# Kernel optimization log

Hardware: AMD Instinct MI355X
Metric: run time of the kernel (lower is better)

## Reference

```python
import jax, jax.numpy as jnp
import numpy as np

N_UNITS = 100
N_INPUTS = 7
N_OUTPUTS = 1
T = 60
STIM_ON, STIM_OFF = 10, 15
RESP_START, RESP_END = 20, 35
REWARD_DURATION = 5
ALPHA = 0.2            # dt / tau = 100 / 500
SIGMA_REC = 0.15
B = 8192


def setup_inputs() -> dict:
    key = jax.random.key(0)
    k1, k2, k3, k4, k5, k6, k7 = jax.random.split(key, 7)
    W_in_raw = (jax.random.normal(k1, (N_UNITS, N_INPUTS)) * 0.05).astype(jnp.float32)
    W_rec_np = np.asarray(jax.random.normal(k2, (N_UNITS, N_UNITS))) / np.sqrt(N_UNITS)
    sr = float(np.abs(np.linalg.eigvals(W_rec_np)).max())
    W_rec = jnp.asarray(W_rec_np * (0.8 / sr), dtype=jnp.float32)
    b_rec = jnp.zeros((N_UNITS,), jnp.float32)
    w_out = (jax.random.normal(k3, (N_OUTPUTS, N_UNITS)) * 0.1).astype(jnp.float32)
    b_out = jnp.zeros((N_OUTPUTS,), jnp.float32)
    return {
        "y0": jnp.zeros((B, N_UNITS), jnp.float32),
        "noise": jax.random.normal(k4, (B, T, N_UNITS), dtype=jnp.float32),
        "stimulus_idx": jax.random.randint(k5, (B,), 0, 4).astype(jnp.int32),
        "rewarded_target_idx": jax.random.randint(k6, (B,), 0, 4).astype(jnp.int32),
        "instruction": jax.random.randint(k7, (B,), 0, 2).astype(jnp.int32),
        "W_in_raw": W_in_raw, "W_rec": W_rec, "b_rec": b_rec,
        "w_out": w_out, "b_out": b_out,
    }


def reference(y0, noise, stimulus_idx, rewarded_target_idx, instruction,
              W_in_raw, W_rec, b_rec, w_out, b_out):
    W_in = jnp.abs(W_in_raw)               # [N, n_in]
    w_lick = W_in[:, 5]
    w_reward = W_in[:, 4]
    noise_scale = SIGMA_REC * float(np.sqrt(2.0 * ALPHA))
    t_idx = jnp.arange(T, dtype=jnp.int32)
    stim_mask = ((t_idx >= STIM_ON) & (t_idx < STIM_OFF)).astype(jnp.float32)
    resp_mask = ((t_idx >= RESP_START) & (t_idx < RESP_END)).astype(jnp.float32)
    auto_start = RESP_END - REWARD_DURATION

    def trial(y0_i, eps_i, stim, rew, instr):
        is_rew = stim == rew
        instr_b = instr > 0
        # base open-loop input: stimulus channel + response cue (channel 6)
        u_base = jnp.zeros((T, N_INPUTS), jnp.float32).at[:, 6].set(resp_mask)
        u_base = u_base + stim_mask[:, None] * jax.nn.one_hot(stim, N_INPUTS, dtype=jnp.float32)
        wu = u_base @ W_in.T + b_rec        # [T, N]

        def step(carry, xs):
            y, licked, lick_t, instr_fired = carry
            t, wu_t, eps_t = xs
            # instruction auto-reward fires at auto_start if no reward yet (applied BEFORE pre)
            delivered = instr_fired | (licked & is_rew)
            fire = instr_b & (~delivered) & (t == auto_start)
            instr_fired = instr_fired | fire
            instr_active = instr_fired & (t >= auto_start) & (t < RESP_END)
            # lick-triggered inputs affect dynamics only AFTER the lick step (wu[t] already consumed)
            lick_dyn = licked & (t > lick_t) & (t < lick_t + REWARD_DURATION)
            add = (instr_active.astype(jnp.float32) + (lick_dyn & is_rew).astype(jnp.float32)) * w_reward \
                  + lick_dyn.astype(jnp.float32) * w_lick
            pre = y @ W_rec.T + wu_t + add + noise_scale * eps_t
            y = (1.0 - ALPHA) * y + ALPHA * jax.nn.relu(pre)
            z = jax.nn.sigmoid(y @ w_out.T + b_out)[0]
            # closed-loop lick decision (after readout)
            in_resp = (t >= RESP_START) & (t < RESP_END)
            trig = in_resp & (~licked) & (z > 0.5)
            lick_t = jnp.where(trig, t, lick_t)
            licked = licked | trig
            # u_trial markings include the lick step itself
            u5 = licked & (t >= lick_t) & (t < lick_t + REWARD_DURATION)
            u4 = instr_active | (u5 & is_rew)
            return (y, licked, lick_t, instr_fired), (z, u5, u4)

        init = (y0_i, jnp.array(False), jnp.array(T + 1, jnp.int32), jnp.array(False))
        (yf, licked, lick_t, instr_fired), (z_seq, u5, u4) = jax.lax.scan(
            step, init, (t_idx, wu, eps_i))
        u = u_base.at[:, 5].set(u5.astype(jnp.float32)).at[:, 4].set(u4.astype(jnp.float32))
        reward_delivered = instr_fired | (licked & is_rew)
        target = jnp.where(is_rew, resp_mask, jnp.zeros_like(resp_mask))
        return u, target, resp_mask > 0, licked, reward_delivered, z_seq, yf

    return jax.vmap(trial)(y0, noise, stimulus_idx, rewarded_target_idx, instruction)
```

## Files before the change

kernel.cpp:

```cpp
#include <hip/hip_runtime.h>
#include <math.h>

#define BB 8192
#define TT 60
#define NU 100
#define NI 7

typedef float v2f __attribute__((ext_vector_type(2)));
typedef float v4f __attribute__((ext_vector_type(4)));

#define FOR50(M) M(0) M(1) M(2) M(3) M(4) M(5) M(6) M(7) M(8) M(9) \
  M(10) M(11) M(12) M(13) M(14) M(15) M(16) M(17) M(18) M(19) \
  M(20) M(21) M(22) M(23) M(24) M(25) M(26) M(27) M(28) M(29) \
  M(30) M(31) M(32) M(33) M(34) M(35) M(36) M(37) M(38) M(39) \
  M(40) M(41) M(42) M(43) M(44) M(45) M(46) M(47) M(48) M(49)

#define FOR25(M) M(0,0,1) M(1,2,3) M(2,4,5) M(3,6,7) M(4,8,9) \
  M(5,10,11) M(6,12,13) M(7,14,15) M(8,16,17) M(9,18,19) \
  M(10,20,21) M(11,22,23) M(12,24,25) M(13,26,27) M(14,28,29) \
  M(15,30,31) M(16,32,33) M(17,34,35) M(18,36,37) M(19,38,39) \
  M(20,40,41) M(21,42,43) M(22,44,45) M(23,46,47) M(24,48,49)

#define DECLW(j) \
  const v2f wa_##j = rowA[j]; \
  const v2f wb_##j = rowB[j];

#define MAC2(j2, ja, jb) { \
  const v4f y4 = Yv[j2]; \
  const v2f ylo = { y4.x, y4.y }; \
  const v2f yhi = { y4.z, y4.w }; \
  accA0 += ylo * wa_##ja; \
  accB0 += ylo * wb_##ja; \
  accA1 += yhi * wa_##jb; \
  accB1 += yhi * wb_##jb; }

#define RL(v,l) __int_as_float(__builtin_amdgcn_readlane(__float_as_int(v), l))

#define DPPADD(ctrl, rmask) { \
  const int _t = __builtin_amdgcn_update_dpp(0, __float_as_int(part), (ctrl), (rmask), 0xf, false); \
  part += __int_as_float(_t); }

__global__ __launch_bounds__(256, 1)
void drr_kernel(const float* __restrict__ y0,
                const float* __restrict__ noise,
                const int*   __restrict__ stim_idx,
                const int*   __restrict__ rew_idx,
                const int*   __restrict__ instr_in,
                const float* __restrict__ W_in_raw,
                const float* __restrict__ W_rec,
                const float* __restrict__ b_rec,
                const float* __restrict__ w_out,
                const float* __restrict__ b_out,
                float* __restrict__ out)
{
    const int lane  = threadIdx.x & 63;
    const int wid   = threadIdx.x >> 6;
    const int trial = blockIdx.x * 4 + wid;

    const bool act = (lane < 50);
    const int  la  = act ? lane : 49;
    const int  ua  = 2 * la;
    const int  uao = ua * NU;

    const int  stim    = stim_idx[trial];
    const int  rew     = rew_idx[trial];
    const bool is_rew  = (stim == rew);
    const bool instr_b = (instr_in[trial] > 0);

    const v2f* rowA = (const v2f*)(W_rec + uao);
    const v2f* rowB = rowA + (NU / 2);
    FOR50(DECLW)

    const v2f wi6 = { fabsf(W_in_raw[ua * NI + 6]),    fabsf(W_in_raw[(ua+1) * NI + 6]) };
    const v2f wis = { fabsf(W_in_raw[ua * NI + stim]), fabsf(W_in_raw[(ua+1) * NI + stim]) };
    const v2f wr  = { fabsf(W_in_raw[ua * NI + 4]),    fabsf(W_in_raw[(ua+1) * NI + 4]) };
    const v2f wl  = { fabsf(W_in_raw[ua * NI + 5]),    fabsf(W_in_raw[(ua+1) * NI + 5]) };
    const v2f br  = { b_rec[ua], b_rec[ua + 1] };
    const v2f wo  = act ? (v2f){ w_out[ua], w_out[ua + 1] } : (v2f){ 0.0f, 0.0f };
    const float bo = b_out[0];

    const v2f* y0v = (const v2f*)(y0 + trial * NU);
    v2f yy = y0v[la];

    const float NS = 0.09486832980505138f;

    bool licked = false, instr_fired = false;
    int  lick_t = TT + 1;

    const float* nbase = noise + trial * (TT * NU);
    v2f en = ((const v2f*)nbase)[la];

    __shared__ v4f lds_y[4][32];
    v2f*       yw = (v2f*)&lds_y[wid][0];
    const v4f* Yv = &lds_y[wid][0];

    float* uout  = out;
    float* tout  = out  + BB * TT * NI;
    float* rout  = tout + BB * TT;
    float* lout  = rout + BB * TT;
    float* dout  = lout + BB;
    float* zout  = dout + BB;
    float* yfout = zout + BB * TT;

    for (int t = 0; t < TT; ++t) {
        yw[la] = yy;

        const v2f e = en;
        if (t < TT - 1)
            en = ((const v2f*)(nbase + (t + 1) * NU))[la];

        const float sm = (t >= 10 && t < 15) ? 1.0f : 0.0f;
        const float rm = (t >= 20 && t < 35) ? 1.0f : 0.0f;

        const bool delivered    = instr_fired || (licked && is_rew);
        const bool fire         = instr_b && !delivered && (t == 30);
        instr_fired             = instr_fired || fire;
        const bool instr_active = instr_fired && (t >= 30) && (t < 35);
        const bool lick_dyn     = licked && (t > lick_t) && (t < lick_t + 5);
        const float a_rew  = (instr_active ? 1.0f : 0.0f) + ((lick_dyn && is_rew) ? 1.0f : 0.0f);
        const float a_lick = lick_dyn ? 1.0f : 0.0f;

        const v2f base = br + rm * wi6 + sm * wis + a_rew * wr + a_lick * wl + NS * e;

        v2f accA0 = { 0.0f, 0.0f };
        v2f accA1 = { 0.0f, 0.0f };
        v2f accB0 = { 0.0f, 0.0f };
        v2f accB1 = { 0.0f, 0.0f };

        FOR25(MAC2)

        const v2f sA  = accA0 + accA1;
        const v2f sB  = accB0 + accB1;
        const v2f pre = base + (v2f){ sA.x + sA.y, sB.x + sB.y };
        const v2f prer = { fmaxf(pre.x, 0.0f), fmaxf(pre.y, 0.0f) };
        yy = 0.8f * yy + 0.2f * prer;

        float part = yy.x * wo.x + yy.y * wo.y;
        DPPADD(0x111, 0xf)
        DPPADD(0x112, 0xf)
        DPPADD(0x114, 0xf)
        DPPADD(0x118, 0xf)
        DPPADD(0x142, 0xa)
        DPPADD(0x143, 0xc)
        const float x = RL(part, 63) + bo;
        const float z = 1.0f / (1.0f + expf(-x));

        const bool in_resp = (t >= 20) && (t < 35);
        const bool trig    = in_resp && !licked && (z > 0.5f);
        if (trig) lick_t = t;
        licked = licked || trig;
        const bool u5 = licked && (t >= lick_t) && (t < lick_t + 5);
        const bool u4 = instr_active || (u5 && is_rew);

        const int bt = trial * TT + t;
        if (lane < NI) {
            float uv = 0.0f;
            if (lane == stim) uv = sm;
            if (lane == 4)    uv = u4 ? 1.0f : 0.0f;
            if (lane == 5)    uv = u5 ? 1.0f : 0.0f;
            if (lane == 6)    uv = rm;
            uout[bt * NI + lane] = uv;
        } else if (lane == 8) {
            tout[bt] = is_rew ? rm : 0.0f;
        } else if (lane == 9) {
            rout[bt] = rm;
        } else if (lane == 10) {
            zout[bt] = z;
        }
    }

    if (lane == 0) {
        lout[trial] = licked ? 1.0f : 0.0f;
        dout[trial] = (instr_fired || (licked && is_rew)) ? 1.0f : 0.0f;
    }
    if (act)
        ((v2f*)(yfout + trial * NU))[la] = yy;
}

extern "C" void kernel_launch(void* const* d_in, const int* in_sizes, int n_in,
                              void* d_out, int out_size, void* d_ws, size_t ws_size,
                              hipStream_t stream) {
    const float* y0       = (const float*)d_in[0];
    const float* noise    = (const float*)d_in[1];
    const int*   stim     = (const int*)  d_in[2];
    const int*   rew      = (const int*)  d_in[3];
    const int*   instr    = (const int*)  d_in[4];
    const float* W_in_raw = (const float*)d_in[5];
    const float* W_rec    = (const float*)d_in[6];
    const float* b_rec    = (const float*)d_in[7];
    const float* w_out    = (const float*)d_in[8];
    const float* b_out    = (const float*)d_in[9];
    float* out = (float*)d_out;

    drr_kernel<<<BB / 4, 256, 0, stream>>>(y0, noise, stim, rew, instr,
                                           W_in_raw, W_rec, b_rec, w_out, b_out, out);
}
```

Before: 519.5 us.

## Split recurrent matvec K-dimension across two waves per trial with LDS exchange

Each trial now uses two wavefronts, each holding half of the W_rec columns (50 instead of 100 per lane-pair), so register pressure drops and launch bounds allow 3 blocks per CU. Partial sums are exchanged through a double-buffered LDS array with a block-wide barrier every timestep, and the y vector is stored rotated so each half reads its own slice. Only one wave of each pair writes outputs. The trade-off is twice the launched waves and one __syncthreads per step on the serial recurrence, in exchange for higher occupancy.

```diff
diff --git a/kernel.cpp b/kernel.cpp
--- a/kernel.cpp
+++ b/kernel.cpp
@@ -9,17 +9,12 @@
 typedef float v2f __attribute__((ext_vector_type(2)));
 typedef float v4f __attribute__((ext_vector_type(4)));
 
-#define FOR50(M) M(0) M(1) M(2) M(3) M(4) M(5) M(6) M(7) M(8) M(9) \
+#define FOR25(M) M(0) M(1) M(2) M(3) M(4) M(5) M(6) M(7) M(8) M(9) \
   M(10) M(11) M(12) M(13) M(14) M(15) M(16) M(17) M(18) M(19) \
-  M(20) M(21) M(22) M(23) M(24) M(25) M(26) M(27) M(28) M(29) \
-  M(30) M(31) M(32) M(33) M(34) M(35) M(36) M(37) M(38) M(39) \
-  M(40) M(41) M(42) M(43) M(44) M(45) M(46) M(47) M(48) M(49)
-
-#define FOR25(M) M(0,0,1) M(1,2,3) M(2,4,5) M(3,6,7) M(4,8,9) \
-  M(5,10,11) M(6,12,13) M(7,14,15) M(8,16,17) M(9,18,19) \
-  M(10,20,21) M(11,22,23) M(12,24,25) M(13,26,27) M(14,28,29) \
-  M(15,30,31) M(16,32,33) M(17,34,35) M(18,36,37) M(19,38,39) \
-  M(20,40,41) M(21,42,43) M(22,44,45) M(23,46,47) M(24,48,49)
+  M(20) M(21) M(22) M(23) M(24)
+
+#define FOR12P(M) M(0,0,1) M(1,2,3) M(2,4,5) M(3,6,7) M(4,8,9) M(5,10,11) \
+  M(6,12,13) M(7,14,15) M(8,16,17) M(9,18,19) M(10,20,21) M(11,22,23)
 
 #define DECLW(j) \
   const v2f wa_##j = rowA[j]; \
@@ -40,7 +35,7 @@
   const int _t = __builtin_amdgcn_update_dpp(0, __float_as_int(part), (ctrl), (rmask), 0xf, false); \
   part += __int_as_float(_t); }
 
-__global__ __launch_bounds__(256, 1)
+__global__ __launch_bounds__(256, 3)
 void drr_kernel(const float* __restrict__ y0,
                 const float* __restrict__ noise,
                 const int*   __restrict__ stim_idx,
@@ -55,7 +50,8 @@
 {
     const int lane  = threadIdx.x & 63;
     const int wid   = threadIdx.x >> 6;
-    const int trial = blockIdx.x * 4 + wid;
+    const int kh    = wid & 1;
+    const int trial = blockIdx.x * 2 + (wid >> 1);
 
     const bool act = (lane < 50);
     const int  la  = act ? lane : 49;
@@ -67,9 +63,9 @@
     const bool is_rew  = (stim == rew);
     const bool instr_b = (instr_in[trial] > 0);
 
-    const v2f* rowA = (const v2f*)(W_rec + uao);
-    const v2f* rowB = rowA + (NU / 2);
-    FOR50(DECLW)
+    const v2f* rowA = (const v2f*)(W_rec + uao + kh * 50);
+    const v2f* rowB = (const v2f*)(W_rec + uao + NU + kh * 50);
+    FOR25(DECLW)
 
     const v2f wi6 = { fabsf(W_in_raw[ua * NI + 6]),    fabsf(W_in_raw[(ua+1) * NI + 6]) };
     const v2f wis = { fabsf(W_in_raw[ua * NI + stim]), fabsf(W_in_raw[(ua+1) * NI + stim]) };
@@ -91,8 +87,12 @@
     v2f en = ((const v2f*)nbase)[la];
 
     __shared__ v4f lds_y[4][32];
+    __shared__ v2f lds_p[2][4][64];
+
     v2f*       yw = (v2f*)&lds_y[wid][0];
     const v4f* Yv = &lds_y[wid][0];
+    const v2f* Yt = (const v2f*)&lds_y[wid][0];
+    const int  ypos = (la + kh * 25) % 50;
 
     float* uout  = out;
     float* tout  = out  + BB * TT * NI;
@@ -103,7 +103,7 @@
     float* yfout = zout + BB * TT;
 
     for (int t = 0; t < TT; ++t) {
-        yw[la] = yy;
+        yw[ypos] = yy;
 
         const v2f e = en;
         if (t < TT - 1)
@@ -127,11 +127,22 @@
         v2f accB0 = { 0.0f, 0.0f };
         v2f accB1 = { 0.0f, 0.0f };
 
-        FOR25(MAC2)
-
-        const v2f sA  = accA0 + accA1;
-        const v2f sB  = accB0 + accB1;
-        const v2f pre = base + (v2f){ sA.x + sA.y, sB.x + sB.y };
+        FOR12P(MAC2)
+        {
+            const v2f yt = Yt[24];
+            accA1 += yt * wa_24;
+            accB1 += yt * wb_24;
+        }
+
+        const v2f sA = accA0 + accA1;
+        const v2f sB = accB0 + accB1;
+        const v2f partial = { sA.x + sA.y, sB.x + sB.y };
+
+        lds_p[t & 1][wid][la] = partial;
+        __syncthreads();
+        const v2f other = lds_p[t & 1][wid ^ 1][la];
+
+        const v2f pre  = base + partial + other;
         const v2f prer = { fmaxf(pre.x, 0.0f), fmaxf(pre.y, 0.0f) };
         yy = 0.8f * yy + 0.2f * prer;
 
@@ -152,29 +163,33 @@
         const bool u5 = licked && (t >= lick_t) && (t < lick_t + 5);
         const bool u4 = instr_active || (u5 && is_rew);
 
-        const int bt = trial * TT + t;
-        if (lane < NI) {
-            float uv = 0.0f;
-            if (lane == stim) uv = sm;
-            if (lane == 4)    uv = u4 ? 1.0f : 0.0f;
-            if (lane == 5)    uv = u5 ? 1.0f : 0.0f;
-            if (lane == 6)    uv = rm;
-            uout[bt * NI + lane] = uv;
-        } else if (lane == 8) {
-            tout[bt] = is_rew ? rm : 0.0f;
-        } else if (lane == 9) {
-            rout[bt] = rm;
-        } else if (lane == 10) {
-            zout[bt] = z;
+        if (kh == 0) {
+            const int bt = trial * TT + t;
+            if (lane < NI) {
+                float uv = 0.0f;
+                if (lane == stim) uv = sm;
+                if (lane == 4)    uv = u4 ? 1.0f : 0.0f;
+                if (lane == 5)    uv = u5 ? 1.0f : 0.0f;
+                if (lane == 6)    uv = rm;
+                uout[bt * NI + lane] = uv;
+            } else if (lane == 8) {
+                tout[bt] = is_rew ? rm : 0.0f;
+            } else if (lane == 9) {
+                rout[bt] = rm;
+            } else if (lane == 10) {
+                zout[bt] = z;
+            }
         }
     }
 
-    if (lane == 0) {
-        lout[trial] = licked ? 1.0f : 0.0f;
-        dout[trial] = (instr_fired || (licked && is_rew)) ? 1.0f : 0.0f;
+    if (kh == 0) {
+        if (lane == 0) {
+            lout[trial] = licked ? 1.0f : 0.0f;
+            dout[trial] = (instr_fired || (licked && is_rew)) ? 1.0f : 0.0f;
+        }
+        if (act)
+            ((v2f*)(yfout + trial * NU))[la] = yy;
     }
-    if (act)
-        ((v2f*)(yfout + trial * NU))[la] = yy;
 }
 
 extern "C" void kernel_launch(void* const* d_in, const int* in_sizes, int n_in,
@@ -192,6 +207,6 @@
     const float* b_out    = (const float*)d_in[9];
     float* out = (float*)d_out;
 
-    drr_kernel<<<BB / 4, 256, 0, stream>>>(y0, noise, stim, rew, instr,
+    drr_kernel<<<BB / 2, 256, 0, stream>>>(y0, noise, stim, rew, instr,
                                            W_in_raw, W_rec, b_rec, w_out, b_out, out);
 }
```

Measured after the change: 635.8 us. +22.4%, slower.

## Process two trials per wavefront and software-pipeline readout with next step

Applied to the files above, without the earlier changes.

Each wavefront now advances two independent trials at once, reusing the register-resident W_rec rows for both. The grid is halved. The sigmoid/lick decision and output stores for step t-1 are deferred and interleaved with step t's matvec, so the serial DPP reduction and readlane latency overlap with independent work. This adds more accumulators and live state per lane, which raises register pressure. It also halves the number of wavefronts, reducing latency hiding through occupancy.

```diff
diff --git a/kernel.cpp b/kernel.cpp
--- a/kernel.cpp
+++ b/kernel.cpp
@@ -8,6 +8,7 @@
 
 typedef float v2f __attribute__((ext_vector_type(2)));
 typedef float v4f __attribute__((ext_vector_type(4)));
+
 
 #define FOR50(M) M(0) M(1) M(2) M(3) M(4) M(5) M(6) M(7) M(8) M(9) \
   M(10) M(11) M(12) M(13) M(14) M(15) M(16) M(17) M(18) M(19) \
@@ -25,20 +26,75 @@
   const v2f wa_##j = rowA[j]; \
   const v2f wb_##j = rowB[j];
 
-#define MAC2(j2, ja, jb) { \
-  const v4f y4 = Yv[j2]; \
-  const v2f ylo = { y4.x, y4.y }; \
-  const v2f yhi = { y4.z, y4.w }; \
-  accA0 += ylo * wa_##ja; \
-  accB0 += ylo * wb_##ja; \
-  accA1 += yhi * wa_##jb; \
-  accB1 += yhi * wb_##jb; }
+#define MACJ(j2, ja, jb) { \
+  const v4f yA4 = YvA[j2]; \
+  const v4f yB4 = YvB[j2]; \
+  acc0A += (v2f){yA4.x, yA4.y} * wa_##ja; \
+  acc1A += (v2f){yA4.x, yA4.y} * wb_##ja; \
+  acc2A += (v2f){yA4.z, yA4.w} * wa_##jb; \
+  acc3A += (v2f){yA4.z, yA4.w} * wb_##jb; \
+  acc0B += (v2f){yB4.x, yB4.y} * wa_##ja; \
+  acc1B += (v2f){yB4.x, yB4.y} * wb_##ja; \
+  acc2B += (v2f){yB4.z, yB4.w} * wa_##jb; \
+  acc3B += (v2f){yB4.z, yB4.w} * wb_##jb; }
 
 #define RL(v,l) __int_as_float(__builtin_amdgcn_readlane(__float_as_int(v), l))
 
 #define DPPADD(ctrl, rmask) { \
   const int _t = __builtin_amdgcn_update_dpp(0, __float_as_int(part), (ctrl), (rmask), 0xf, false); \
   part += __int_as_float(_t); }
+
+#define ROUTE(S, t, sm, rm) { \
+  const bool dl = fired##S || (licked##S && isrew##S); \
+  const bool fr = instrb##S && !dl && ((t) == 30); \
+  fired##S = fired##S || fr; \
+  ia##S = fired##S && ((t) >= 30) && ((t) < 35); \
+  const bool ld = licked##S && ((t) > lickt##S) && ((t) < lickt##S + 5); \
+  const float ar = (ia##S ? 1.0f : 0.0f) + ((ld && isrew##S) ? 1.0f : 0.0f); \
+  const float al = ld ? 1.0f : 0.0f; \
+  base##S = br + (rm) * wi6 + (sm) * wis##S + ar * wr + al * wl + NS * e##S; }
+
+#define FINZ(S, tp) { \
+  zz##S = 1.0f / (1.0f + expf(-x##S)); \
+  const bool inr = ((tp) >= 20) && ((tp) < 35); \
+  const bool trig = inr && !licked##S && (zz##S > 0.5f); \
+  if (trig) lickt##S = (tp); \
+  licked##S = licked##S || trig; \
+  u5##S = licked##S && ((tp) >= lickt##S) && ((tp) < lickt##S + 5); \
+  u4##S = ia##S || (u5##S && isrew##S); }
+
+#define UPDATE(S) { \
+  const v2f s0 = acc0##S + acc2##S; \
+  const v2f s1 = acc1##S + acc3##S; \
+  const v2f pre = base##S + (v2f){ s0.x + s0.y, s1.x + s1.y }; \
+  const v2f prer = { fmaxf(pre.x, 0.0f), fmaxf(pre.y, 0.0f) }; \
+  yy##S = 0.8f * yy##S + 0.2f * prer; \
+  yw##S[la] = yy##S; }
+
+#define START(S) { \
+  float part = yy##S.x * wo.x + yy##S.y * wo.y; \
+  DPPADD(0x111, 0xf) \
+  DPPADD(0x112, 0xf) \
+  DPPADD(0x114, 0xf) \
+  DPPADD(0x118, 0xf) \
+  DPPADD(0x142, 0xa) \
+  DPPADD(0x143, 0xc) \
+  x##S = RL(part, 63) + bo; }
+
+#define FSTORE(S, tp) { \
+  const float smp = ((tp) >= 10 && (tp) < 15) ? 1.0f : 0.0f; \
+  const float rmp = ((tp) >= 20 && (tp) < 35) ? 1.0f : 0.0f; \
+  const int bt = trial##S * TT + (tp); \
+  if (lane < NI) { \
+    float uv = 0.0f; \
+    if (lane == stim##S) uv = smp; \
+    if (lane == 4) uv = u4##S ? 1.0f : 0.0f; \
+    if (lane == 5) uv = u5##S ? 1.0f : 0.0f; \
+    if (lane == 6) uv = rmp; \
+    uout[bt * NI + lane] = uv; \
+  } else if (lane == 8) { tout[bt] = isrew##S ? rmp : 0.0f; } \
+  else if (lane == 9)   { rout[bt] = rmp; } \
+  else if (lane == 10)  { zout[bt] = zz##S; } }
 
 __global__ __launch_bounds__(256, 1)
 void drr_kernel(const float* __restrict__ y0,
@@ -55,44 +111,54 @@
 {
     const int lane  = threadIdx.x & 63;
     const int wid   = threadIdx.x >> 6;
-    const int trial = blockIdx.x * 4 + wid;
+    const int trialA = blockIdx.x * 8 + wid * 2;
+    const int trialB = trialA + 1;
 
     const bool act = (lane < 50);
     const int  la  = act ? lane : 49;
     const int  ua  = 2 * la;
     const int  uao = ua * NU;
 
-    const int  stim    = stim_idx[trial];
-    const int  rew     = rew_idx[trial];
-    const bool is_rew  = (stim == rew);
-    const bool instr_b = (instr_in[trial] > 0);
+    const int  stimA  = stim_idx[trialA];
+    const int  stimB  = stim_idx[trialB];
+    const bool isrewA = (stimA == rew_idx[trialA]);
+    const bool isrewB = (stimB == rew_idx[trialB]);
+    const bool instrbA = (instr_in[trialA] > 0);
+    const bool instrbB = (instr_in[trialB] > 0);
 
     const v2f* rowA = (const v2f*)(W_rec + uao);
     const v2f* rowB = rowA + (NU / 2);
     FOR50(DECLW)
 
-    const v2f wi6 = { fabsf(W_in_raw[ua * NI + 6]),    fabsf(W_in_raw[(ua+1) * NI + 6]) };
-    const v2f wis = { fabsf(W_in_raw[ua * NI + stim]), fabsf(W_in_raw[(ua+1) * NI + stim]) };
-    const v2f wr  = { fabsf(W_in_raw[ua * NI + 4]),    fabsf(W_in_raw[(ua+1) * NI + 4]) };
-    const v2f wl  = { fabsf(W_in_raw[ua * NI + 5]),    fabsf(W_in_raw[(ua+1) * NI + 5]) };
-    const v2f br  = { b_rec[ua], b_rec[ua + 1] };
-    const v2f wo  = act ? (v2f){ w_out[ua], w_out[ua + 1] } : (v2f){ 0.0f, 0.0f };
+    const v2f wi6  = { fabsf(W_in_raw[ua * NI + 6]),     fabsf(W_in_raw[(ua+1) * NI + 6]) };
+    const v2f wisA = { fabsf(W_in_raw[ua * NI + stimA]), fabsf(W_in_raw[(ua+1) * NI + stimA]) };
+    const v2f wisB = { fabsf(W_in_raw[ua * NI + stimB]), fabsf(W_in_raw[(ua+1) * NI + stimB]) };
+    const v2f wr   = { fabsf(W_in_raw[ua * NI + 4]),     fabsf(W_in_raw[(ua+1) * NI + 4]) };
+    const v2f wl   = { fabsf(W_in_raw[ua * NI + 5]),     fabsf(W_in_raw[(ua+1) * NI + 5]) };
+    const v2f br   = { b_rec[ua], b_rec[ua + 1] };
+    const v2f wo   = act ? (v2f){ w_out[ua], w_out[ua + 1] } : (v2f){ 0.0f, 0.0f };
     const float bo = b_out[0];
 
-    const v2f* y0v = (const v2f*)(y0 + trial * NU);
-    v2f yy = y0v[la];
+    v2f yyA = ((const v2f*)(y0 + trialA * NU))[la];
+    v2f yyB = ((const v2f*)(y0 + trialB * NU))[la];
 
     const float NS = 0.09486832980505138f;
 
-    bool licked = false, instr_fired = false;
-    int  lick_t = TT + 1;
-
-    const float* nbase = noise + trial * (TT * NU);
-    v2f en = ((const v2f*)nbase)[la];
-
-    __shared__ v4f lds_y[4][32];
-    v2f*       yw = (v2f*)&lds_y[wid][0];
-    const v4f* Yv = &lds_y[wid][0];
+    bool lickedA = false, firedA = false, iaA = false;
+    bool lickedB = false, firedB = false, iaB = false;
+    int  licktA = TT + 1, licktB = TT + 1;
+    float xA = 0.0f, xB = 0.0f;
+
+    const float* nbaseA = noise + trialA * (TT * NU);
+    const float* nbaseB = noise + trialB * (TT * NU);
+    v2f enA = ((const v2f*)nbaseA)[la];
+    v2f enB = ((const v2f*)nbaseB)[la];
+
+    __shared__ v4f lds_y[4][2][32];
+    v2f*       ywA = (v2f*)&lds_y[wid][0][0];
+    v2f*       ywB = (v2f*)&lds_y[wid][1][0];
+    const v4f* YvA = &lds_y[wid][0][0];
+    const v4f* YvB = &lds_y[wid][1][0];
 
     float* uout  = out;
     float* tout  = out  + BB * TT * NI;
@@ -102,79 +168,80 @@
     float* zout  = dout + BB;
     float* yfout = zout + BB * TT;
 
-    for (int t = 0; t < TT; ++t) {
-        yw[la] = yy;
-
-        const v2f e = en;
-        if (t < TT - 1)
-            en = ((const v2f*)(nbase + (t + 1) * NU))[la];
+    ywA[la] = yyA;
+    ywB[la] = yyB;
+
+    {
+        const v2f eA = enA;
+        const v2f eB = enB;
+        enA = ((const v2f*)(nbaseA + NU))[la];
+        enB = ((const v2f*)(nbaseB + NU))[la];
+
+        v2f acc0A = {0,0}, acc1A = {0,0}, acc2A = {0,0}, acc3A = {0,0};
+        v2f acc0B = {0,0}, acc1B = {0,0}, acc2B = {0,0}, acc3B = {0,0};
+        v2f baseA, baseB;
+
+        FOR25(MACJ)
+
+        ROUTE(A, 0, 0.0f, 0.0f)
+        ROUTE(B, 0, 0.0f, 0.0f)
+        UPDATE(A)
+        UPDATE(B)
+        START(A)
+        START(B)
+    }
+
+#pragma unroll 2
+    for (int t = 1; t < TT; ++t) {
+        const v2f eA = enA;
+        const v2f eB = enB;
+        const int tn = (t < TT - 1) ? t + 1 : t;
+        enA = ((const v2f*)(nbaseA + tn * NU))[la];
+        enB = ((const v2f*)(nbaseB + tn * NU))[la];
+
+        v2f acc0A = {0,0}, acc1A = {0,0}, acc2A = {0,0}, acc3A = {0,0};
+        v2f acc0B = {0,0}, acc1B = {0,0}, acc2B = {0,0}, acc3B = {0,0};
+        v2f baseA, baseB;
+        float zzA, zzB;
+        bool u4A, u5A, u4B, u5B;
+
+        FOR25(MACJ)
+
+        FINZ(A, t - 1)
+        FINZ(B, t - 1)
 
         const float sm = (t >= 10 && t < 15) ? 1.0f : 0.0f;
         const float rm = (t >= 20 && t < 35) ? 1.0f : 0.0f;
-
-        const bool delivered    = instr_fired || (licked && is_rew);
-        const bool fire         = instr_b && !delivered && (t == 30);
-        instr_fired             = instr_fired || fire;
-        const bool instr_active = instr_fired && (t >= 30) && (t < 35);
-        const bool lick_dyn     = licked && (t > lick_t) && (t < lick_t + 5);
-        const float a_rew  = (instr_active ? 1.0f : 0.0f) + ((lick_dyn && is_rew) ? 1.0f : 0.0f);
-        const float a_lick = lick_dyn ? 1.0f : 0.0f;
-
-        const v2f base = br + rm * wi6 + sm * wis + a_rew * wr + a_lick * wl + NS * e;
-
-        v2f accA0 = { 0.0f, 0.0f };
-        v2f accA1 = { 0.0f, 0.0f };
-        v2f accB0 = { 0.0f, 0.0f };
-        v2f accB1 = { 0.0f, 0.0f };
-
-        FOR25(MAC2)
-
-        const v2f sA  = accA0 + accA1;
-        const v2f sB  = accB0 + accB1;
-        const v2f pre = base + (v2f){ sA.x + sA.y, sB.x + sB.y };
-        const v2f prer = { fmaxf(pre.x, 0.0f), fmaxf(pre.y, 0.0f) };
-        yy = 0.8f * yy + 0.2f * prer;
-
-        float part = yy.x * wo.x + yy.y * wo.y;
-        DPPADD(0x111, 0xf)
-        DPPADD(0x112, 0xf)
-        DPPADD(0x114, 0xf)
-        DPPADD(0x118, 0xf)
-        DPPADD(0x142, 0xa)
-        DPPADD(0x143, 0xc)
-        const float x = RL(part, 63) + bo;
-        const float z = 1.0f / (1.0f + expf(-x));
-
-        const bool in_resp = (t >= 20) && (t < 35);
-        const bool trig    = in_resp && !licked && (z > 0.5f);
-        if (trig) lick_t = t;
-        licked = licked || trig;
-        const bool u5 = licked && (t >= lick_t) && (t < lick_t + 5);
-        const bool u4 = instr_active || (u5 && is_rew);
-
-        const int bt = trial * TT + t;
-        if (lane < NI) {
-            float uv = 0.0f;
-            if (lane == stim) uv = sm;
-            if (lane == 4)    uv = u4 ? 1.0f : 0.0f;
-            if (lane == 5)    uv = u5 ? 1.0f : 0.0f;
-            if (lane == 6)    uv = rm;
-            uout[bt * NI + lane] = uv;
-        } else if (lane == 8) {
-            tout[bt] = is_rew ? rm : 0.0f;
-        } else if (lane == 9) {
-            rout[bt] = rm;
-        } else if (lane == 10) {
-            zout[bt] = z;
-        }
+        ROUTE(A, t, sm, rm)
+        ROUTE(B, t, sm, rm)
+        UPDATE(A)
+        UPDATE(B)
+        START(A)
+        START(B)
+
+        FSTORE(A, t - 1)
+        FSTORE(B, t - 1)
+    }
+
+    {
+        float zzA, zzB;
+        bool u4A, u5A, u4B, u5B;
+        FINZ(A, TT - 1)
+        FINZ(B, TT - 1)
+        FSTORE(A, TT - 1)
+        FSTORE(B, TT - 1)
     }
 
     if (lane == 0) {
-        lout[trial] = licked ? 1.0f : 0.0f;
-        dout[trial] = (instr_fired || (licked && is_rew)) ? 1.0f : 0.0f;
-    }
-    if (act)
-        ((v2f*)(yfout + trial * NU))[la] = yy;
+        lout[trialA] = lickedA ? 1.0f : 0.0f;
+        dout[trialA] = (firedA || (lickedA && isrewA)) ? 1.0f : 0.0f;
+        lout[trialB] = lickedB ? 1.0f : 0.0f;
+        dout[trialB] = (firedB || (lickedB && isrewB)) ? 1.0f : 0.0f;
+    }
+    if (act) {
+        ((v2f*)(yfout + trialA * NU))[la] = yyA;
+        ((v2f*)(yfout + trialB * NU))[la] = yyB;
+    }
 }
 
 extern "C" void kernel_launch(void* const* d_in, const int* in_sizes, int n_in,
@@ -192,6 +259,6 @@
     const float* b_out    = (const float*)d_in[9];
     float* out = (float*)d_out;
 
-    drr_kernel<<<BB / 4, 256, 0, stream>>>(y0, noise, stim, rew, instr,
+    drr_kernel<<<BB / 8, 256, 0, stream>>>(y0, noise, stim, rew, instr,
                                            W_in_raw, W_rec, b_rec, w_out, b_out, out);
 }
```

New measurement: 832.4 us. 60.2% more time.
